# Kernel tuning notes

Hardware: AMD Instinct MI355X
Metric: run time of the kernel (lower is better)

Reference implementation:

```python
import jax, jax.numpy as jnp
import numpy as np

MAXHD, MAXV, MINA, MAXA, DT = 100.0, 40.0, -6.0, 4.0, 0.1
NVEH, NT, IN_DIM, UNITS = 4096, 1024, 12, 20


def setup_inputs() -> dict:
    key = jax.random.key(0)
    ks = jax.random.split(key, 12)
    leadfol_inputs = jax.random.normal(ks[0], (NVEH, NT, IN_DIM), dtype=jnp.float32)
    init_state = jax.random.normal(ks[1], (NVEH, 2), dtype=jnp.float32)
    hidden_states = jnp.zeros((2, NVEH, UNITS), dtype=jnp.float32)
    s = 0.1
    return {
        "leadfol_inputs": leadfol_inputs,
        "init_state": init_state,
        "hidden_states": hidden_states,
        "kernel": s * jax.random.normal(ks[2], (IN_DIM, 4 * UNITS), dtype=jnp.float32),
        "rkernel": s * jax.random.normal(ks[3], (UNITS, 4 * UNITS), dtype=jnp.float32),
        "bias": jnp.zeros((4 * UNITS,), dtype=jnp.float32),
        "W2": s * jax.random.normal(ks[4], (UNITS, 10), dtype=jnp.float32),
        "b2": jnp.zeros((10,), dtype=jnp.float32),
        "Wlc": s * jax.random.normal(ks[5], (10, 3), dtype=jnp.float32),
        "blc": jnp.zeros((3,), dtype=jnp.float32),
        "W1": s * jax.random.normal(ks[6], (10, 1), dtype=jnp.float32),
        "b1": jnp.zeros((1,), dtype=jnp.float32),
    }


def reference(leadfol_inputs, init_state, hidden_states, kernel, rkernel, bias,
              W2, b2, Wlc, blc, W1, b1):
    # time-major for scan: (nt, nveh, 12)
    xs = jnp.transpose(leadfol_inputs, (1, 0, 2))
    pos0, spd0 = init_state[:, 0], init_state[:, 1]
    h0, c0 = hidden_states[0], hidden_states[1]

    def step(carry, x_t):
        pos, spd, h, c = carry
        lead_hd = (x_t[:, :3] - pos[:, None]) / MAXHD
        fol_hd = (pos[:, None] - x_t[:, 3:6]) / MAXHD
        spds = x_t[:, 6:] / MAXV
        inp = jnp.concatenate([lead_hd, fol_hd, spds], axis=1)  # (nveh, 12)
        inp = jnp.where(jnp.isnan(inp), jnp.ones_like(inp), inp)
        # Keras LSTMCell (inference, no dropout): gate order i, f, g, o
        z = inp @ kernel + h @ rkernel + bias
        i_g, f_g, g_g, o_g = jnp.split(z, 4, axis=1)
        c_new = jax.nn.sigmoid(f_g) * c + jax.nn.sigmoid(i_g) * jnp.tanh(g_g)
        h_new = jax.nn.sigmoid(o_g) * jnp.tanh(c_new)
        x2 = jax.nn.relu(h_new @ W2 + b2)          # (nveh, 10)
        lc = x2 @ Wlc + blc                          # (nveh, 3)
        acc_raw = (x2 @ W1 + b1)[:, 0]               # (nveh,)
        acc = (MAXA - MINA) * acc_raw + MINA
        pos_new = pos + DT * spd
        spd_new = spd + DT * acc
        return (pos_new, spd_new, h_new, c_new), (pos_new, lc)

    (pos_f, spd_f, h_f, c_f), (traj, lc_all) = jax.lax.scan(step, (pos0, spd0, h0, c0), xs)
    pred_traj = jnp.transpose(traj, (1, 0))            # (nveh, nt)
    pred_lc_action = jnp.transpose(lc_all, (1, 0, 2))  # (nveh, nt, 3)
    return pred_traj, pred_lc_action, spd_f, (h_f, c_f)
```

## Files before the change

kernel.cpp:

```cpp
#include <hip/hip_runtime.h>
#include <cstdint>

#define NVEH  4096
#define NT    1024
#define INW   12
#define UNITS 20

typedef float f32x2 __attribute__((ext_vector_type(2)));

#define PIN(v)  asm volatile("" : "+v"(v))

#define PKFMA_LO(acc, w, s2) \
    asm("v_pk_fma_f32 %0, %1, %2, %0 op_sel:[0,0,0] op_sel_hi:[1,0,1]" \
        : "+v"(acc) : "v"(w), "v"(s2))
#define PKFMA_HI(acc, w, s2) \
    asm("v_pk_fma_f32 %0, %1, %2, %0 op_sel:[0,1,0] op_sel_hi:[1,1,1]" \
        : "+v"(acc) : "v"(w), "v"(s2))
#define PKMUL_LO(dst, w, s2) \
    asm("v_pk_mul_f32 %0, %1, %2 op_sel:[0,0] op_sel_hi:[1,0]" \
        : "=v"(dst) : "v"(w), "v"(s2))
#define PKMUL_HI(acc, w, s2) \
    asm("v_pk_fma_f32 %0, %1, %2, %0 op_sel:[0,1,0] op_sel_hi:[1,1,1]" \
        : "+v"(acc) : "v"(w), "v"(s2))

__device__ __forceinline__ float fexp2(float x) { return __builtin_amdgcn_exp2f(x); }
__device__ __forceinline__ float frcp(float x)  { return __builtin_amdgcn_rcpf(x); }

__global__ __attribute__((amdgpu_waves_per_eu(2, 2))) __launch_bounds__(64)
void rnncf_kernel(const float* __restrict__ x,
                  const float* __restrict__ init_state,
                  const float* __restrict__ hs,
                  const float* __restrict__ K,
                  const float* __restrict__ R,
                  const float* __restrict__ bias,
                  const float* __restrict__ W2,
                  const float* __restrict__ b2,
                  const float* __restrict__ Wlc,
                  const float* __restrict__ blc,
                  const float* __restrict__ W1,
                  const float* __restrict__ b1,
                  float* __restrict__ out)
{
    const int lane = threadIdx.x;
    const int grp  = lane / 20;
    const int sub  = lane % 20;
    const int veh  = blockIdx.x * 3 + grp;
    const bool active = (grp < 3) && (veh < NVEH);
    const int vs = active ? veh : 0;

    __shared__ __align__(16) float x_lds[2][4][12];
    __shared__ __align__(16) float h_lds[4][20];
    __shared__ __align__(16) float x2_lds[4][12];

    const float s01l = -1.4426950408889634f;
    const float s01h = -1.4426950408889634f;
    const float s23l =  2.8853900817779268f;
    const float s23h = -1.4426950408889634f;
    f32x2 K01[12], K23[12], R01[20], R23[20], bz01, bz23;
    bz01[0] = s01l * bias[sub];      bz01[1] = s01h * bias[20 + sub];
    bz23[0] = s23l * bias[40 + sub]; bz23[1] = s23h * bias[60 + sub];
#pragma unroll
    for (int k = 0; k < 12; ++k) {
        K01[k][0] = s01l * K[k * 80 + sub];      K01[k][1] = s01h * K[k * 80 + 20 + sub];
        K23[k][0] = s23l * K[k * 80 + 40 + sub]; K23[k][1] = s23h * K[k * 80 + 60 + sub];
    }
#pragma unroll
    for (int k = 0; k < 20; ++k) {
        R01[k][0] = s01l * R[k * 80 + sub];      R01[k][1] = s01h * R[k * 80 + 20 + sub];
        R23[k][0] = s23l * R[k * 80 + 40 + sub]; R23[k][1] = s23h * R[k * 80 + 60 + sub];
    }
    const int mh = (sub < 10) ? sub : 9;
    f32x2 W2p[10];
#pragma unroll
    for (int u = 0; u < 10; ++u) {
        W2p[u][0] = W2[(2 * u) * 10 + mh];
        W2p[u][1] = W2[(2 * u + 1) * 10 + mh];
    }
    float b2s = b2[mh];
    const int jl = (sub < 3) ? sub : 0;
    f32x2 Wlcp[5];
#pragma unroll
    for (int m = 0; m < 5; ++m) {
        Wlcp[m][0] = Wlc[(2 * m) * 3 + jl];
        Wlcp[m][1] = Wlc[(2 * m + 1) * 3 + jl];
    }
    float blcs = blc[jl];
    PIN(bz01); PIN(bz23);
#pragma unroll
    for (int k = 0; k < 12; ++k) { PIN(K01[k]); PIN(K23[k]); }
#pragma unroll
    for (int k = 0; k < 20; ++k) { PIN(R01[k]); PIN(R23[k]); }
#pragma unroll
    for (int u = 0; u < 10; ++u) PIN(W2p[u]);
#pragma unroll
    for (int m = 0; m < 5; ++m) PIN(Wlcp[m]);
    PIN(b2s); PIN(blcs);

    float pos = init_state[vs * 2 + 0];
    float spd = init_state[vs * 2 + 1];
    float c   = hs[(size_t)NVEH * UNITS + (size_t)vs * UNITS + sub];
    float hnew = hs[(size_t)vs * UNITS + sub];

    h_lds[grp][sub] = hnew;
    __builtin_amdgcn_wave_barrier();
    f32x2 hrp[10];
#pragma unroll
    for (int q = 0; q < 5; ++q) {
        float4 v = ((const float4*)&h_lds[grp][0])[q];
        hrp[2*q][0]   = v.x; hrp[2*q][1]   = v.y;
        hrp[2*q+1][0] = v.z; hrp[2*q+1][1] = v.w;
    }
    __builtin_amdgcn_wave_barrier();

    const bool ldx = active && (sub < 3);
    const float4* xrow = (const float4*)(x + (size_t)vs * NT * INW) + sub;
    float4 v0  = ldx ? xrow[0]     : float4{0,0,0,0};
    float4 xfA = ldx ? xrow[3]     : float4{0,0,0,0};
    float4 xfB = ldx ? xrow[2*3]   : float4{0,0,0,0};
    if (sub < 3) ((float4*)&x_lds[0][grp][0])[sub] = v0;
    __builtin_amdgcn_wave_barrier();

    float* trajp = out + (size_t)vs * NT;
    float* lcp   = out + (size_t)NVEH * NT + (size_t)vs * NT * 3;

    float xm = 0.0f;

    for (int t = 0; t < NT; ++t) {
        float4 u0 = ((const float4*)&x_lds[t & 1][grp][0])[0];
        float4 u1 = ((const float4*)&x_lds[t & 1][grp][0])[1];
        float4 u2 = ((const float4*)&x_lds[t & 1][grp][0])[2];
        f32x2 x2p[5];
        if (t > 0) {
#pragma unroll
            for (int q = 0; q < 5; ++q)
                x2p[q] = ((const f32x2*)&x2_lds[grp][0])[q];
        }
        __builtin_amdgcn_wave_barrier();

        if (sub < 3) ((float4*)&x_lds[(t + 1) & 1][grp][0])[sub] = xfA;
        xfA = xfB;
        {
            int tt = t + 3; if (tt > NT - 1) tt = NT - 1;
            if (ldx) xfB = xrow[tt * 3];
        }

        const float pp = pos * 0.01f;
        f32x2 inp2[6];
        inp2[0][0] = fmaf(u0.x,  0.01f, -pp); inp2[0][1] = fmaf(u0.y,  0.01f, -pp);
        inp2[1][0] = fmaf(u0.z,  0.01f, -pp); inp2[1][1] = fmaf(u0.w, -0.01f,  pp);
        inp2[2][0] = fmaf(u1.x, -0.01f,  pp); inp2[2][1] = fmaf(u1.y, -0.01f,  pp);
        inp2[3][0] = u1.z * 0.025f;           inp2[3][1] = u1.w * 0.025f;
        inp2[4][0] = u2.x * 0.025f;           inp2[4][1] = u2.y * 0.025f;
        inp2[5][0] = u2.z * 0.025f;           inp2[5][1] = u2.w * 0.025f;

        f32x2 zK01 = bz01, zK23 = bz23;
#pragma unroll
        for (int j = 0; j < 6; ++j) {
            PKFMA_LO(zK01, K01[2*j],   inp2[j]);
            PKFMA_LO(zK23, K23[2*j],   inp2[j]);
            PKFMA_HI(zK01, K01[2*j+1], inp2[j]);
            PKFMA_HI(zK23, K23[2*j+1], inp2[j]);
        }
        f32x2 zA01, zA23, zB01, zB23;
        PKMUL_LO(zA01, R01[0], hrp[0]);
        PKMUL_LO(zA23, R23[0], hrp[0]);
        PKMUL_HI(zA01, R01[1], hrp[0]);
        PKMUL_HI(zA23, R23[1], hrp[0]);
#pragma unroll
        for (int j = 1; j < 5; ++j) {
            PKFMA_LO(zA01, R01[2*j],   hrp[j]);
            PKFMA_LO(zA23, R23[2*j],   hrp[j]);
            PKFMA_HI(zA01, R01[2*j+1], hrp[j]);
            PKFMA_HI(zA23, R23[2*j+1], hrp[j]);
        }
        PKMUL_LO(zB01, R01[10], hrp[5]);
        PKMUL_LO(zB23, R23[10], hrp[5]);
        PKMUL_HI(zB01, R01[11], hrp[5]);
        PKMUL_HI(zB23, R23[11], hrp[5]);
#pragma unroll
        for (int j = 6; j < 10; ++j) {
            PKFMA_LO(zB01, R01[2*j],   hrp[j]);
            PKFMA_LO(zB23, R23[2*j],   hrp[j]);
            PKFMA_HI(zB01, R01[2*j+1], hrp[j]);
            PKFMA_HI(zB23, R23[2*j+1], hrp[j]);
        }
        f32x2 z01 = (zK01 + zA01) + zB01;
        f32x2 z23 = (zK23 + zA23) + zB23;

        if (t > 0) {
            f32x2 ac2; ac2[0] = b1[0]; ac2[1] = 0.0f;
#pragma unroll
            for (int m = 0; m < 5; ++m) {
                ac2[0] = fmaf(x2p[m][0], W1[2*m],   ac2[0]);
                ac2[1] = fmaf(x2p[m][1], W1[2*m+1], ac2[1]);
            }
            float accr = ac2[0] + ac2[1];
            spd = fmaf(0.1f, fmaf(10.0f, accr, -6.0f), spd);
            if (active && sub < 3) {
                f32x2 lc2; lc2[0] = blcs; lc2[1] = 0.0f;
#pragma unroll
                for (int m = 0; m < 5; ++m) {
                    lc2[0] = fmaf(x2p[m][0], Wlcp[m][0], lc2[0]);
                    lc2[1] = fmaf(x2p[m][1], Wlcp[m][1], lc2[1]);
                }
                lcp[(t - 1) * 3 + sub] = lc2[0] + lc2[1];
            }
        }

        float ig = frcp(1.0f + fexp2(z01[0]));
        float fg = frcp(1.0f + fexp2(z01[1]));
        float gg = 1.0f - 2.0f * frcp(fexp2(z23[0]) + 1.0f);
        float og = frcp(1.0f + fexp2(z23[1]));
        c = fmaf(fg, c, ig * gg);
        float th = 1.0f - 2.0f * frcp(fexp2(2.8853900817779268f * c) + 1.0f);
        hnew = og * th;

        float posn = fmaf(0.1f, spd, pos);
        if (active && sub == 0) trajp[t] = posn;
        pos = posn;

        h_lds[grp][sub] = hnew;
        __builtin_amdgcn_wave_barrier();
#pragma unroll
        for (int q = 0; q < 5; ++q) {
            float4 v = ((const float4*)&h_lds[grp][0])[q];
            hrp[2*q][0]   = v.x; hrp[2*q][1]   = v.y;
            hrp[2*q+1][0] = v.z; hrp[2*q+1][1] = v.w;
        }
        __builtin_amdgcn_wave_barrier();

        f32x2 xm2; xm2[0] = b2s; xm2[1] = 0.0f;
#pragma unroll
        for (int u = 0; u < 10; ++u) {
            xm2[0] = fmaf(hrp[u][0], W2p[u][0], xm2[0]);
            xm2[1] = fmaf(hrp[u][1], W2p[u][1], xm2[1]);
        }
        xm = fmaxf(xm2[0] + xm2[1], 0.0f);
        if (sub < 10) x2_lds[grp][sub] = xm;
        __builtin_amdgcn_wave_barrier();
    }

    {
        f32x2 x2p[5];
#pragma unroll
        for (int q = 0; q < 5; ++q)
            x2p[q] = ((const f32x2*)&x2_lds[grp][0])[q];
        f32x2 ac2; ac2[0] = b1[0]; ac2[1] = 0.0f;
#pragma unroll
        for (int m = 0; m < 5; ++m) {
            ac2[0] = fmaf(x2p[m][0], W1[2*m],   ac2[0]);
            ac2[1] = fmaf(x2p[m][1], W1[2*m+1], ac2[1]);
        }
        float accr = ac2[0] + ac2[1];
        spd = fmaf(0.1f, fmaf(10.0f, accr, -6.0f), spd);
        if (active && sub < 3) {
            f32x2 lc2; lc2[0] = blcs; lc2[1] = 0.0f;
#pragma unroll
            for (int m = 0; m < 5; ++m) {
                lc2[0] = fmaf(x2p[m][0], Wlcp[m][0], lc2[0]);
                lc2[1] = fmaf(x2p[m][1], Wlcp[m][1], lc2[1]);
            }
            lcp[(NT - 1) * 3 + sub] = lc2[0] + lc2[1];
        }
    }

    if (active) {
        float* spdf = out + (size_t)NVEH * NT * 4;
        float* hf   = spdf + NVEH;
        float* cf   = hf + (size_t)NVEH * UNITS;
        if (sub == 0) spdf[veh] = spd;
        hf[(size_t)veh * UNITS + sub] = hnew;
        cf[(size_t)veh * UNITS + sub] = c;
    }
}

extern "C" void kernel_launch(void* const* d_in, const int* in_sizes, int n_in,
                              void* d_out, int out_size, void* d_ws, size_t ws_size,
                              hipStream_t stream) {
    const float* x    = (const float*)d_in[0];
    const float* st0  = (const float*)d_in[1];
    const float* hs   = (const float*)d_in[2];
    const float* K    = (const float*)d_in[3];
    const float* R    = (const float*)d_in[4];
    const float* bias = (const float*)d_in[5];
    const float* W2   = (const float*)d_in[6];
    const float* b2   = (const float*)d_in[7];
    const float* Wlc  = (const float*)d_in[8];
    const float* blc  = (const float*)d_in[9];
    const float* W1   = (const float*)d_in[10];
    const float* b1   = (const float*)d_in[11];
    float* out = (float*)d_out;

    dim3 grid((NVEH + 2) / 3);
    dim3 block(64);
    hipLaunchKernelGGL(rnncf_kernel, grid, block, 0, stream,
                       x, st0, hs, K, R, bias, W2, b2, Wlc, blc, W1, b1, out);
}
```

Measured before the change: 710.6 us.

## Stage inputs via async global-to-LDS loads in an 8-deep ring, pack small FMAs

Replaces the register-prefetch double buffer of input rows with direct global_load_lds transfers into an 8-slot LDS ring. Nine lanes each issue one 16-byte load per timestep, and the main loop is unrolled by 4 with one vmcnt wait per block. It also keeps W1 in registers and uses packed FMAs for the W2, W1 and Wlc dot products. The aim is to take global-load latency and the register-to-LDS copies off the serial recurrence path. The risks are that the vmcnt count can be thrown off by the interleaved global stores, and that the async LDS writes are not explicitly ordered against the LDS reads.

```diff
diff --git a/kernel.cpp b/kernel.cpp
--- a/kernel.cpp
+++ b/kernel.cpp
@@ -19,12 +19,18 @@
 #define PKMUL_LO(dst, w, s2) \
     asm("v_pk_mul_f32 %0, %1, %2 op_sel:[0,0] op_sel_hi:[1,0]" \
         : "=v"(dst) : "v"(w), "v"(s2))
-#define PKMUL_HI(acc, w, s2) \
-    asm("v_pk_fma_f32 %0, %1, %2, %0 op_sel:[0,1,0] op_sel_hi:[1,1,1]" \
-        : "+v"(acc) : "v"(w), "v"(s2))
+#define PKFMA(acc, a, b) \
+    asm("v_pk_fma_f32 %0, %1, %2, %0" : "+v"(acc) : "v"(a), "v"(b))
 
 __device__ __forceinline__ float fexp2(float x) { return __builtin_amdgcn_exp2f(x); }
 __device__ __forceinline__ float frcp(float x)  { return __builtin_amdgcn_rcpf(x); }
+
+__device__ __forceinline__ void gload_lds16(const float* g, float* l) {
+    __builtin_amdgcn_global_load_lds(
+        (const __attribute__((address_space(1))) unsigned int*)g,
+        (__attribute__((address_space(3))) unsigned int*)l,
+        16, 0, 0);
+}
 
 __global__ __attribute__((amdgpu_waves_per_eu(2, 2))) __launch_bounds__(64)
 void rnncf_kernel(const float* __restrict__ x,
@@ -48,7 +54,7 @@
     const bool active = (grp < 3) && (veh < NVEH);
     const int vs = active ? veh : 0;
 
-    __shared__ __align__(16) float x_lds[2][4][12];
+    __shared__ __align__(16) float x_lds[8][4][12];
     __shared__ __align__(16) float h_lds[4][20];
     __shared__ __align__(16) float x2_lds[4][12];
 
@@ -85,6 +91,9 @@
         Wlcp[m][1] = Wlc[(2 * m + 1) * 3 + jl];
     }
     float blcs = blc[jl];
+    f32x2 W1p[5];
+#pragma unroll
+    for (int m = 0; m < 5; ++m) { W1p[m][0] = W1[2 * m]; W1p[m][1] = W1[2 * m + 1]; }
     PIN(bz01); PIN(bz23);
 #pragma unroll
     for (int k = 0; k < 12; ++k) { PIN(K01[k]); PIN(K23[k]); }
@@ -93,7 +102,7 @@
 #pragma unroll
     for (int u = 0; u < 10; ++u) PIN(W2p[u]);
 #pragma unroll
-    for (int m = 0; m < 5; ++m) PIN(Wlcp[m]);
+    for (int m = 0; m < 5; ++m) { PIN(Wlcp[m]); PIN(W1p[m]); }
     PIN(b2s); PIN(blcs);
 
     float pos = init_state[vs * 2 + 0];
@@ -112,132 +121,134 @@
     }
     __builtin_amdgcn_wave_barrier();
 
-    const bool ldx = active && (sub < 3);
-    const float4* xrow = (const float4*)(x + (size_t)vs * NT * INW) + sub;
-    float4 v0  = ldx ? xrow[0]     : float4{0,0,0,0};
-    float4 xfA = ldx ? xrow[3]     : float4{0,0,0,0};
-    float4 xfB = ldx ? xrow[2*3]   : float4{0,0,0,0};
-    if (sub < 3) ((float4*)&x_lds[0][grp][0])[sub] = v0;
-    __builtin_amdgcn_wave_barrier();
+    const bool stg = (lane < 9);
+    int sveh = blockIdx.x * 3 + lane / 3;
+    if (sveh > NVEH - 1) sveh = NVEH - 1;
+    const float* sgp = x + (size_t)sveh * NT * INW + (lane % 3) * 4;
+
+    if (stg) {
+#pragma unroll
+        for (int t0 = 0; t0 < 8; ++t0)
+            gload_lds16(sgp + (size_t)t0 * INW, &x_lds[t0][0][0]);
+    }
 
     float* trajp = out + (size_t)vs * NT;
     float* lcp   = out + (size_t)NVEH * NT + (size_t)vs * NT * 3;
 
     float xm = 0.0f;
 
-    for (int t = 0; t < NT; ++t) {
-        float4 u0 = ((const float4*)&x_lds[t & 1][grp][0])[0];
-        float4 u1 = ((const float4*)&x_lds[t & 1][grp][0])[1];
-        float4 u2 = ((const float4*)&x_lds[t & 1][grp][0])[2];
-        f32x2 x2p[5];
-        if (t > 0) {
-#pragma unroll
-            for (int q = 0; q < 5; ++q)
-                x2p[q] = ((const f32x2*)&x2_lds[grp][0])[q];
+    for (int tb = 0; tb < NT; tb += 4) {
+        asm volatile("s_waitcnt vmcnt(4)" ::: "memory");
+
+#pragma unroll
+        for (int j = 0; j < 4; ++j) {
+            const int t = tb + j;
+
+            float4 u0 = ((const float4*)&x_lds[t & 7][grp][0])[0];
+            float4 u1 = ((const float4*)&x_lds[t & 7][grp][0])[1];
+            float4 u2 = ((const float4*)&x_lds[t & 7][grp][0])[2];
+            f32x2 x2p[5];
+            if (t > 0) {
+#pragma unroll
+                for (int q = 0; q < 5; ++q)
+                    x2p[q] = ((const f32x2*)&x2_lds[grp][0])[q];
+            }
+            __builtin_amdgcn_wave_barrier();
+
+            const float pp = pos * 0.01f;
+            f32x2 inp2[6];
+            inp2[0][0] = fmaf(u0.x,  0.01f, -pp); inp2[0][1] = fmaf(u0.y,  0.01f, -pp);
+            inp2[1][0] = fmaf(u0.z,  0.01f, -pp); inp2[1][1] = fmaf(u0.w, -0.01f,  pp);
+            inp2[2][0] = fmaf(u1.x, -0.01f,  pp); inp2[2][1] = fmaf(u1.y, -0.01f,  pp);
+            inp2[3][0] = u1.z * 0.025f;           inp2[3][1] = u1.w * 0.025f;
+            inp2[4][0] = u2.x * 0.025f;           inp2[4][1] = u2.y * 0.025f;
+            inp2[5][0] = u2.z * 0.025f;           inp2[5][1] = u2.w * 0.025f;
+
+            f32x2 zK01 = bz01, zK23 = bz23;
+#pragma unroll
+            for (int q = 0; q < 6; ++q) {
+                PKFMA_LO(zK01, K01[2*q],   inp2[q]);
+                PKFMA_LO(zK23, K23[2*q],   inp2[q]);
+                PKFMA_HI(zK01, K01[2*q+1], inp2[q]);
+                PKFMA_HI(zK23, K23[2*q+1], inp2[q]);
+            }
+            f32x2 zA01, zA23, zB01, zB23;
+            PKMUL_LO(zA01, R01[0], hrp[0]);
+            PKMUL_LO(zA23, R23[0], hrp[0]);
+            PKFMA_HI(zA01, R01[1], hrp[0]);
+            PKFMA_HI(zA23, R23[1], hrp[0]);
+#pragma unroll
+            for (int q = 1; q < 5; ++q) {
+                PKFMA_LO(zA01, R01[2*q],   hrp[q]);
+                PKFMA_LO(zA23, R23[2*q],   hrp[q]);
+                PKFMA_HI(zA01, R01[2*q+1], hrp[q]);
+                PKFMA_HI(zA23, R23[2*q+1], hrp[q]);
+            }
+            PKMUL_LO(zB01, R01[10], hrp[5]);
+            PKMUL_LO(zB23, R23[10], hrp[5]);
+            PKFMA_HI(zB01, R01[11], hrp[5]);
+            PKFMA_HI(zB23, R23[11], hrp[5]);
+#pragma unroll
+            for (int q = 6; q < 10; ++q) {
+                PKFMA_LO(zB01, R01[2*q],   hrp[q]);
+                PKFMA_LO(zB23, R23[2*q],   hrp[q]);
+                PKFMA_HI(zB01, R01[2*q+1], hrp[q]);
+                PKFMA_HI(zB23, R23[2*q+1], hrp[q]);
+            }
+            f32x2 z01 = (zK01 + zA01) + zB01;
+            f32x2 z23 = (zK23 + zA23) + zB23;
+
+            if (t > 0) {
+                f32x2 ac2; ac2[0] = b1[0]; ac2[1] = 0.0f;
+#pragma unroll
+                for (int m = 0; m < 5; ++m) PKFMA(ac2, x2p[m], W1p[m]);
+                float accr = ac2[0] + ac2[1];
+                spd = fmaf(0.1f, fmaf(10.0f, accr, -6.0f), spd);
+                if (active && sub < 3) {
+                    f32x2 lc2; lc2[0] = blcs; lc2[1] = 0.0f;
+#pragma unroll
+                    for (int m = 0; m < 5; ++m) PKFMA(lc2, x2p[m], Wlcp[m]);
+                    lcp[(t - 1) * 3 + sub] = lc2[0] + lc2[1];
+                }
+            }
+
+            float ig = frcp(1.0f + fexp2(z01[0]));
+            float fg = frcp(1.0f + fexp2(z01[1]));
+            float gg = 1.0f - 2.0f * frcp(fexp2(z23[0]) + 1.0f);
+            float og = frcp(1.0f + fexp2(z23[1]));
+            c = fmaf(fg, c, ig * gg);
+            float th = 1.0f - 2.0f * frcp(fexp2(2.8853900817779268f * c) + 1.0f);
+            hnew = og * th;
+
+            float posn = fmaf(0.1f, spd, pos);
+            if (active && sub == 0) trajp[t] = posn;
+            pos = posn;
+
+            h_lds[grp][sub] = hnew;
+            __builtin_amdgcn_wave_barrier();
+#pragma unroll
+            for (int q = 0; q < 5; ++q) {
+                float4 v = ((const float4*)&h_lds[grp][0])[q];
+                hrp[2*q][0]   = v.x; hrp[2*q][1]   = v.y;
+                hrp[2*q+1][0] = v.z; hrp[2*q+1][1] = v.w;
+            }
+            __builtin_amdgcn_wave_barrier();
+
+            f32x2 xm2; xm2[0] = b2s; xm2[1] = 0.0f;
+#pragma unroll
+            for (int u = 0; u < 10; ++u) PKFMA(xm2, hrp[u], W2p[u]);
+            xm = fmaxf(xm2[0] + xm2[1], 0.0f);
+            if (sub < 10) x2_lds[grp][sub] = xm;
+            __builtin_amdgcn_wave_barrier();
         }
-        __builtin_amdgcn_wave_barrier();
-
-        if (sub < 3) ((float4*)&x_lds[(t + 1) & 1][grp][0])[sub] = xfA;
-        xfA = xfB;
-        {
-            int tt = t + 3; if (tt > NT - 1) tt = NT - 1;
-            if (ldx) xfB = xrow[tt * 3];
+
+        if (stg) {
+#pragma unroll
+            for (int j = 0; j < 4; ++j) {
+                int tt = tb + 8 + j; if (tt > NT - 1) tt = NT - 1;
+                gload_lds16(sgp + (size_t)tt * INW, &x_lds[(tb + j) & 7][0][0]);
+            }
         }
-
-        const float pp = pos * 0.01f;
-        f32x2 inp2[6];
-        inp2[0][0] = fmaf(u0.x,  0.01f, -pp); inp2[0][1] = fmaf(u0.y,  0.01f, -pp);
-        inp2[1][0] = fmaf(u0.z,  0.01f, -pp); inp2[1][1] = fmaf(u0.w, -0.01f,  pp);
-        inp2[2][0] = fmaf(u1.x, -0.01f,  pp); inp2[2][1] = fmaf(u1.y, -0.01f,  pp);
-        inp2[3][0] = u1.z * 0.025f;           inp2[3][1] = u1.w * 0.025f;
-        inp2[4][0] = u2.x * 0.025f;           inp2[4][1] = u2.y * 0.025f;
-        inp2[5][0] = u2.z * 0.025f;           inp2[5][1] = u2.w * 0.025f;
-
-        f32x2 zK01 = bz01, zK23 = bz23;
-#pragma unroll
-        for (int j = 0; j < 6; ++j) {
-            PKFMA_LO(zK01, K01[2*j],   inp2[j]);
-            PKFMA_LO(zK23, K23[2*j],   inp2[j]);
-            PKFMA_HI(zK01, K01[2*j+1], inp2[j]);
-            PKFMA_HI(zK23, K23[2*j+1], inp2[j]);
-        }
-        f32x2 zA01, zA23, zB01, zB23;
-        PKMUL_LO(zA01, R01[0], hrp[0]);
-        PKMUL_LO(zA23, R23[0], hrp[0]);
-        PKMUL_HI(zA01, R01[1], hrp[0]);
-        PKMUL_HI(zA23, R23[1], hrp[0]);
-#pragma unroll
-        for (int j = 1; j < 5; ++j) {
-            PKFMA_LO(zA01, R01[2*j],   hrp[j]);
-            PKFMA_LO(zA23, R23[2*j],   hrp[j]);
-            PKFMA_HI(zA01, R01[2*j+1], hrp[j]);
-            PKFMA_HI(zA23, R23[2*j+1], hrp[j]);
-        }
-        PKMUL_LO(zB01, R01[10], hrp[5]);
-        PKMUL_LO(zB23, R23[10], hrp[5]);
-        PKMUL_HI(zB01, R01[11], hrp[5]);
-        PKMUL_HI(zB23, R23[11], hrp[5]);
-#pragma unroll
-        for (int j = 6; j < 10; ++j) {
-            PKFMA_LO(zB01, R01[2*j],   hrp[j]);
-            PKFMA_LO(zB23, R23[2*j],   hrp[j]);
-            PKFMA_HI(zB01, R01[2*j+1], hrp[j]);
-            PKFMA_HI(zB23, R23[2*j+1], hrp[j]);
-        }
-        f32x2 z01 = (zK01 + zA01) + zB01;
-        f32x2 z23 = (zK23 + zA23) + zB23;
-
-        if (t > 0) {
-            f32x2 ac2; ac2[0] = b1[0]; ac2[1] = 0.0f;
-#pragma unroll
-            for (int m = 0; m < 5; ++m) {
-                ac2[0] = fmaf(x2p[m][0], W1[2*m],   ac2[0]);
-                ac2[1] = fmaf(x2p[m][1], W1[2*m+1], ac2[1]);
-            }
-            float accr = ac2[0] + ac2[1];
-            spd = fmaf(0.1f, fmaf(10.0f, accr, -6.0f), spd);
-            if (active && sub < 3) {
-                f32x2 lc2; lc2[0] = blcs; lc2[1] = 0.0f;
-#pragma unroll
-                for (int m = 0; m < 5; ++m) {
-                    lc2[0] = fmaf(x2p[m][0], Wlcp[m][0], lc2[0]);
-                    lc2[1] = fmaf(x2p[m][1], Wlcp[m][1], lc2[1]);
-                }
-                lcp[(t - 1) * 3 + sub] = lc2[0] + lc2[1];
-            }
-        }
-
-        float ig = frcp(1.0f + fexp2(z01[0]));
-        float fg = frcp(1.0f + fexp2(z01[1]));
-        float gg = 1.0f - 2.0f * frcp(fexp2(z23[0]) + 1.0f);
-        float og = frcp(1.0f + fexp2(z23[1]));
-        c = fmaf(fg, c, ig * gg);
-        float th = 1.0f - 2.0f * frcp(fexp2(2.8853900817779268f * c) + 1.0f);
-        hnew = og * th;
-
-        float posn = fmaf(0.1f, spd, pos);
-        if (active && sub == 0) trajp[t] = posn;
-        pos = posn;
-
-        h_lds[grp][sub] = hnew;
-        __builtin_amdgcn_wave_barrier();
-#pragma unroll
-        for (int q = 0; q < 5; ++q) {
-            float4 v = ((const float4*)&h_lds[grp][0])[q];
-            hrp[2*q][0]   = v.x; hrp[2*q][1]   = v.y;
-            hrp[2*q+1][0] = v.z; hrp[2*q+1][1] = v.w;
-        }
-        __builtin_amdgcn_wave_barrier();
-
-        f32x2 xm2; xm2[0] = b2s; xm2[1] = 0.0f;
-#pragma unroll
-        for (int u = 0; u < 10; ++u) {
-            xm2[0] = fmaf(hrp[u][0], W2p[u][0], xm2[0]);
-            xm2[1] = fmaf(hrp[u][1], W2p[u][1], xm2[1]);
-        }
-        xm = fmaxf(xm2[0] + xm2[1], 0.0f);
-        if (sub < 10) x2_lds[grp][sub] = xm;
-        __builtin_amdgcn_wave_barrier();
     }
 
     {
@@ -247,19 +258,13 @@
             x2p[q] = ((const f32x2*)&x2_lds[grp][0])[q];
         f32x2 ac2; ac2[0] = b1[0]; ac2[1] = 0.0f;
 #pragma unroll
-        for (int m = 0; m < 5; ++m) {
-            ac2[0] = fmaf(x2p[m][0], W1[2*m],   ac2[0]);
-            ac2[1] = fmaf(x2p[m][1], W1[2*m+1], ac2[1]);
-        }
+        for (int m = 0; m < 5; ++m) PKFMA(ac2, x2p[m], W1p[m]);
         float accr = ac2[0] + ac2[1];
         spd = fmaf(0.1f, fmaf(10.0f, accr, -6.0f), spd);
         if (active && sub < 3) {
             f32x2 lc2; lc2[0] = blcs; lc2[1] = 0.0f;
 #pragma unroll
-            for (int m = 0; m < 5; ++m) {
-                lc2[0] = fmaf(x2p[m][0], Wlcp[m][0], lc2[0]);
-                lc2[1] = fmaf(x2p[m][1], Wlcp[m][1], lc2[1]);
-            }
+            for (int m = 0; m < 5; ++m) PKFMA(lc2, x2p[m], Wlcp[m]);
             lcp[(NT - 1) * 3 + sub] = lc2[0] + lc2[1];
         }
     }
```

Measured after the change: 690.3 us. 1.03x faster.
